# Kernel optimization log

Measured on AMD Instinct MI355X. Metric: run time of the kernel, lower is better.

## Reference

```python
import jax, jax.numpy as jnp
import numpy as np

N_NODES = 10000
IN_DIM, EDGE_DIM, HID_DIM, OUT_DIM = 128, 64, 256, 128
N_EDGES = 640000


def setup_inputs() -> dict:
    key = jax.random.key(0)
    ks = jax.random.split(key, 8)
    x = jax.random.normal(ks[0], (N_NODES, IN_DIM), dtype=jnp.float32)
    edge_index = jax.random.randint(ks[1], (2, N_EDGES), 0, N_NODES, dtype=jnp.int64)
    edge_attr = jax.random.normal(ks[2], (N_EDGES, EDGE_DIM), dtype=jnp.float32)
    # MLP params (PyTorch Linear: y = x @ W.T + b), Kaiming-uniform-ish scale
    s1 = 1.0 / np.sqrt(IN_DIM + EDGE_DIM)
    s2 = 1.0 / np.sqrt(HID_DIM)
    W1 = jax.random.uniform(ks[3], (HID_DIM, IN_DIM + EDGE_DIM), minval=-s1, maxval=s1, dtype=jnp.float32)
    b1 = jax.random.uniform(ks[4], (HID_DIM,), minval=-s1, maxval=s1, dtype=jnp.float32)
    W2 = jax.random.uniform(ks[5], (OUT_DIM, HID_DIM), minval=-s2, maxval=s2, dtype=jnp.float32)
    b2 = jax.random.uniform(ks[6], (OUT_DIM,), minval=-s2, maxval=s2, dtype=jnp.float32)
    return {"x": x, "edge_index": edge_index, "edge_attr": edge_attr,
            "W1": W1, "b1": b1, "W2": W2, "b2": b2}


def reference(x, edge_index, edge_attr, W1, b1, W2, b2):
    # GINE-style concat-message conv: gather -> per-edge MLP -> scatter-add.
    src = edge_index[0]  # message source node x_j
    dst = edge_index[1]  # aggregation target node
    m = jnp.concatenate([x[src], edge_attr], axis=-1)         # [E, F+Fe]
    h = jax.nn.relu(m @ W1.T + b1)                            # [E, H]
    msg = h @ W2.T + b2                                       # [E, O]
    out = jax.ops.segment_sum(msg, dst, num_segments=x.shape[0])  # [N, O]
    return out
```

## Files before the change

kernel.cpp:

```cpp
#include <hip/hip_runtime.h>

#define N_NODES 10000
#define IN_DIM 128
#define EDGE_DIM 64
#define HID_DIM 256
#define OUT_DIM 128
#define N_EDGES 640000


typedef __bf16 bf16x8 __attribute__((ext_vector_type(8)));
typedef float f32x4 __attribute__((ext_vector_type(4)));

static __device__ __forceinline__ unsigned short f2bf(float f) {
    unsigned u = __builtin_bit_cast(unsigned, f);
    u = (u + 0x7fffu + ((u >> 16) & 1u)) >> 16;
    return (unsigned short)u;
}

__global__ void zero_kernel(float* __restrict__ out) {
    int t = blockIdx.x * 256 + threadIdx.x;
    if (t < 320000) ((float4*)out)[t] = make_float4(0.f, 0.f, 0.f, 0.f);
}

__global__ __launch_bounds__(256, 2) void gine_hybrid(
    const int* __restrict__ ei,
    const float* __restrict__ x,
    const float* __restrict__ ea,
    const float* __restrict__ W1,
    const float* __restrict__ b1,
    const float* __restrict__ W2,
    const float* __restrict__ b2,
    float* __restrict__ out)
{
    __shared__ unsigned        sW1u[128 * 97];
    __shared__ __align__(16) float sMsg[16 * 132];
    __shared__ unsigned short  sHu[16 * 132];
    __shared__ float           sB1[128];
    __shared__ int             sSE[16], sDE[16];

    unsigned* sMu = (unsigned*)sMsg;

    const int tid  = threadIdx.x;
    const int hb   = blockIdx.x & 1;
    const int bseq = blockIdx.x >> 1;

    for (int i = tid; i < 128 * 96; i += 256) {
        int r = i / 96, c2 = i - r * 96;
        const float* wr = W1 + (hb * 128 + r) * 192 + c2 * 2;
        sW1u[r * 97 + c2] = (unsigned)f2bf(wr[0]) | ((unsigned)f2bf(wr[1]) << 16);
    }
    if (tid < 128) sB1[tid] = b1[hb * 128 + tid];

    const int o    = tid & 127;
    const int lane = tid & 63;
    const int e16  = lane & 15;
    const int q    = lane >> 4;
    const int wv   = tid >> 6;

    bf16x8 w2frag[2][4];
    #pragma unroll
    for (int mtl = 0; mtl < 2; ++mtl) {
        const float* wbase = W2 + (size_t)((wv * 2 + mtl) * 16 + e16) * 256 + hb * 128 + q * 8;
        #pragma unroll
        for (int kb = 0; kb < 4; ++kb) {
            const float* wr = wbase + kb * 32;
            int4 ai;
            ai.x = (int)((unsigned)f2bf(wr[0]) | ((unsigned)f2bf(wr[1]) << 16));
            ai.y = (int)((unsigned)f2bf(wr[2]) | ((unsigned)f2bf(wr[3]) << 16));
            ai.z = (int)((unsigned)f2bf(wr[4]) | ((unsigned)f2bf(wr[5]) << 16));
            ai.w = (int)((unsigned)f2bf(wr[6]) | ((unsigned)f2bf(wr[7]) << 16));
            w2frag[mtl][kb] = __builtin_bit_cast(bf16x8, ai);
        }
    }
    const float b2o = (hb == 0) ? b2[o] : 0.f;

    __syncthreads();

    for (int g = bseq; g < 40000; g += 512) {
        if (tid < 16) {
            sSE[tid] = ei[g * 16 + tid];
            sDE[tid] = ei[N_EDGES + g * 16 + tid];
        }
        __syncthreads();

        for (int i = tid; i < 16 * 48; i += 256) {
            int ee = i / 48, c4 = i - ee * 48;
            int k = c4 * 4;
            float4 v;
            if (k < 128) v = *(const float4*)(x + (size_t)sSE[ee] * 128 + k);
            else         v = *(const float4*)(ea + (size_t)(g * 16 + ee) * 64 + (k - 128));
            unsigned* mp = sMu + ee * 97 + c4 * 2;
            mp[0] = (unsigned)f2bf(v.x) | ((unsigned)f2bf(v.y) << 16);
            mp[1] = (unsigned)f2bf(v.z) | ((unsigned)f2bf(v.w) << 16);
        }
        __syncthreads();

        {
            f32x4 acc[2];
            acc[0] = (f32x4){0.f, 0.f, 0.f, 0.f};
            acc[1] = (f32x4){0.f, 0.f, 0.f, 0.f};
            #pragma unroll
            for (int ks = 0; ks < 6; ++ks) {
                const unsigned* mp = sMu + e16 * 97 + ks * 16 + q * 4;
                int4 bi;
                bi.x = (int)mp[0]; bi.y = (int)mp[1];
                bi.z = (int)mp[2]; bi.w = (int)mp[3];
                bf16x8 bfrag = __builtin_bit_cast(bf16x8, bi);
                #pragma unroll
                for (int mtl = 0; mtl < 2; ++mtl) {
                    const unsigned* ap = sW1u + ((wv * 2 + mtl) * 16 + e16) * 97 + ks * 16 + q * 4;
                    int4 ai;
                    ai.x = (int)ap[0]; ai.y = (int)ap[1];
                    ai.z = (int)ap[2]; ai.w = (int)ap[3];
                    bf16x8 afrag = __builtin_bit_cast(bf16x8, ai);
                    acc[mtl] = __builtin_amdgcn_mfma_f32_16x16x32_bf16(afrag, bfrag, acc[mtl], 0, 0, 0);
                }
            }
            #pragma unroll
            for (int mtl = 0; mtl < 2; ++mtl) {
                const int hid = (wv * 2 + mtl) * 16 + q * 4;
                float v0 = fmaxf(acc[mtl][0] + sB1[hid + 0], 0.f);
                float v1 = fmaxf(acc[mtl][1] + sB1[hid + 1], 0.f);
                float v2 = fmaxf(acc[mtl][2] + sB1[hid + 2], 0.f);
                float v3 = fmaxf(acc[mtl][3] + sB1[hid + 3], 0.f);
                unsigned* hp = ((unsigned*)sHu) + e16 * 66 + (hid >> 1);
                hp[0] = (unsigned)f2bf(v0) | ((unsigned)f2bf(v1) << 16);
                hp[1] = (unsigned)f2bf(v2) | ((unsigned)f2bf(v3) << 16);
            }
        }
        __syncthreads();

        {
            f32x4 acc2[2];
            acc2[0] = (f32x4){0.f, 0.f, 0.f, 0.f};
            acc2[1] = (f32x4){0.f, 0.f, 0.f, 0.f};
            #pragma unroll
            for (int kb = 0; kb < 4; ++kb) {
                const unsigned* hp = ((const unsigned*)sHu) + e16 * 66 + kb * 16 + q * 4;
                int4 bi;
                bi.x = (int)hp[0]; bi.y = (int)hp[1];
                bi.z = (int)hp[2]; bi.w = (int)hp[3];
                bf16x8 bfrag = __builtin_bit_cast(bf16x8, bi);
                acc2[0] = __builtin_amdgcn_mfma_f32_16x16x32_bf16(w2frag[0][kb], bfrag, acc2[0], 0, 0, 0);
                acc2[1] = __builtin_amdgcn_mfma_f32_16x16x32_bf16(w2frag[1][kb], bfrag, acc2[1], 0, 0, 0);
            }
            #pragma unroll
            for (int mtl = 0; mtl < 2; ++mtl) {
                float* mp = sMsg + e16 * 132 + (wv * 2 + mtl) * 16 + q * 4;
                mp[0] = acc2[mtl][0]; mp[1] = acc2[mtl][1];
                mp[2] = acc2[mtl][2]; mp[3] = acc2[mtl][3];
            }
        }
        __syncthreads();

        {
            const int eb = (tid >> 7) * 8;
            #pragma unroll
            for (int q2 = 0; q2 < 8; ++q2) {
                int ee = eb + q2;
                float v = sMsg[ee * 132 + o] + b2o;
                unsafeAtomicAdd(out + (size_t)sDE[ee] * 128 + o, v);
            }
        }
        __syncthreads();
    }
}

extern "C" void kernel_launch(void* const* d_in, const int* in_sizes, int n_in,
                              void* d_out, int out_size, void* d_ws, size_t ws_size,
                              hipStream_t stream) {
    const float* x  = (const float*)d_in[0];
    const int*   ei = (const int*)d_in[1];
    const float* ea = (const float*)d_in[2];
    const float* W1 = (const float*)d_in[3];
    const float* b1 = (const float*)d_in[4];
    const float* W2 = (const float*)d_in[5];
    const float* b2 = (const float*)d_in[6];
    float* out = (float*)d_out;

    zero_kernel<<<1250, 256, 0, stream>>>(out);
    gine_hybrid<<<1024, 256, 0, stream>>>(ei, x, ea, W1, b1, W2, b2, out);
}
```

Baseline: 884.2 us.

## Double-buffer edge gathers in LDS and cut per-group block barriers

Restructures the edge-group loop into a software pipeline. The next group's x/edge_attr rows and the group after next's edge indices are loaded into registers during the current group's MLP and written to a second LDS buffer afterwards. This hides gather latency and reduces block barriers per group from five to two, since each wave reads back only its own sMsg columns. LDS rows are XOR-swizzled instead of padded, fragments are loaded with vector int4 reads, and fp32-to-bf16 packing for inputs and weights now truncates instead of rounding, which slightly lowers accuracy.

```diff
diff --git a/kernel.cpp b/kernel.cpp
--- a/kernel.cpp
+++ b/kernel.cpp
@@ -11,6 +11,10 @@
 typedef __bf16 bf16x8 __attribute__((ext_vector_type(8)));
 typedef float f32x4 __attribute__((ext_vector_type(4)));
 
+static __device__ __forceinline__ unsigned pk_pre(float lo, float hi) {
+    return (__builtin_bit_cast(unsigned, lo) >> 16) |
+           (__builtin_bit_cast(unsigned, hi) & 0xFFFF0000u);
+}
 static __device__ __forceinline__ unsigned short f2bf(float f) {
     unsigned u = __builtin_bit_cast(unsigned, f);
     u = (u + 0x7fffu + ((u >> 16) & 1u)) >> 16;
@@ -22,7 +26,12 @@
     if (t < 320000) ((float4*)out)[t] = make_float4(0.f, 0.f, 0.f, 0.f);
 }
 
-__global__ __launch_bounds__(256, 2) void gine_hybrid(
+#define FENCE_LGKM()  asm volatile("s_waitcnt lgkmcnt(0)" ::: "memory")
+#define SCHED_FENCE() __builtin_amdgcn_sched_barrier(0)
+#define BLOCK_BAR()   do { FENCE_LGKM(); SCHED_FENCE(); \
+                           __builtin_amdgcn_s_barrier(); SCHED_FENCE(); } while (0)
+
+__global__ __launch_bounds__(256, 2) void gine_pipe(
     const int* __restrict__ ei,
     const float* __restrict__ x,
     const float* __restrict__ ea,
@@ -32,13 +41,12 @@
     const float* __restrict__ b2,
     float* __restrict__ out)
 {
-    __shared__ unsigned        sW1u[128 * 97];
-    __shared__ __align__(16) float sMsg[16 * 132];
-    __shared__ unsigned short  sHu[16 * 132];
-    __shared__ float           sB1[128];
-    __shared__ int             sSE[16], sDE[16];
-
-    unsigned* sMu = (unsigned*)sMsg;
+    __shared__ __align__(16) unsigned sW1u[128 * 96];
+    __shared__ __align__(16) unsigned sMu[2][16 * 96];
+    __shared__ __align__(16) unsigned sHuU[16 * 64];
+    __shared__ __align__(16) float    sMsg[16 * 132];
+    __shared__ float sB1[128];
+    __shared__ __align__(16) int sSE[2][16], sDE[2][16];
 
     const int tid  = threadIdx.x;
     const int hb   = blockIdx.x & 1;
@@ -46,16 +54,19 @@
 
     for (int i = tid; i < 128 * 96; i += 256) {
         int r = i / 96, c2 = i - r * 96;
-        const float* wr = W1 + (hb * 128 + r) * 192 + c2 * 2;
-        sW1u[r * 97 + c2] = (unsigned)f2bf(wr[0]) | ((unsigned)f2bf(wr[1]) << 16);
+        const float* w = W1 + (size_t)(hb * 128 + r) * 192 + c2 * 2;
+        sW1u[r * 96 + (c2 ^ ((r & 7) << 2))] = pk_pre(w[0], w[1]);
     }
     if (tid < 128) sB1[tid] = b1[hb * 128 + tid];
 
-    const int o    = tid & 127;
     const int lane = tid & 63;
     const int e16  = lane & 15;
     const int q    = lane >> 4;
     const int wv   = tid >> 6;
+    const int l32  = lane & 31;
+    const int eh   = (lane >> 5) * 8;
+    const int o    = wv * 32 + l32;
+    const int rsw  = (e16 & 7) << 2;
 
     bf16x8 w2frag[2][4];
     #pragma unroll
@@ -65,104 +76,133 @@
         for (int kb = 0; kb < 4; ++kb) {
             const float* wr = wbase + kb * 32;
             int4 ai;
-            ai.x = (int)((unsigned)f2bf(wr[0]) | ((unsigned)f2bf(wr[1]) << 16));
-            ai.y = (int)((unsigned)f2bf(wr[2]) | ((unsigned)f2bf(wr[3]) << 16));
-            ai.z = (int)((unsigned)f2bf(wr[4]) | ((unsigned)f2bf(wr[5]) << 16));
-            ai.w = (int)((unsigned)f2bf(wr[6]) | ((unsigned)f2bf(wr[7]) << 16));
+            ai.x = (int)pk_pre(wr[0], wr[1]);
+            ai.y = (int)pk_pre(wr[2], wr[3]);
+            ai.z = (int)pk_pre(wr[4], wr[5]);
+            ai.w = (int)pk_pre(wr[6], wr[7]);
             w2frag[mtl][kb] = __builtin_bit_cast(bf16x8, ai);
         }
     }
-    const float b2o = (hb == 0) ? b2[o] : 0.f;
-
+    const float b2o = hb ? 0.f : b2[o];
+
+    {
+        const int g0 = bseq;
+        const int g1 = (bseq + 512 < 40000) ? bseq + 512 : bseq;
+        if (tid < 16) {
+            sSE[0][tid] = ei[g0 * 16 + tid];
+            sDE[0][tid] = ei[N_EDGES + g0 * 16 + tid];
+        } else if (tid < 32) {
+            int t = tid - 16;
+            sSE[1][t] = ei[g1 * 16 + t];
+            sDE[1][t] = ei[N_EDGES + g1 * 16 + t];
+        }
+    }
     __syncthreads();
 
-    for (int g = bseq; g < 40000; g += 512) {
-        if (tid < 16) {
-            sSE[tid] = ei[g * 16 + tid];
-            sDE[tid] = ei[N_EDGES + g * 16 + tid];
-        }
-        __syncthreads();
-
-        for (int i = tid; i < 16 * 48; i += 256) {
-            int ee = i / 48, c4 = i - ee * 48;
-            int k = c4 * 4;
-            float4 v;
-            if (k < 128) v = *(const float4*)(x + (size_t)sSE[ee] * 128 + k);
-            else         v = *(const float4*)(ea + (size_t)(g * 16 + ee) * 64 + (k - 128));
-            unsigned* mp = sMu + ee * 97 + c4 * 2;
-            mp[0] = (unsigned)f2bf(v.x) | ((unsigned)f2bf(v.y) << 16);
-            mp[1] = (unsigned)f2bf(v.z) | ((unsigned)f2bf(v.w) << 16);
-        }
-        __syncthreads();
-
-        {
-            f32x4 acc[2];
-            acc[0] = (f32x4){0.f, 0.f, 0.f, 0.f};
-            acc[1] = (f32x4){0.f, 0.f, 0.f, 0.f};
-            #pragma unroll
-            for (int ks = 0; ks < 6; ++ks) {
-                const unsigned* mp = sMu + e16 * 97 + ks * 16 + q * 4;
-                int4 bi;
-                bi.x = (int)mp[0]; bi.y = (int)mp[1];
-                bi.z = (int)mp[2]; bi.w = (int)mp[3];
-                bf16x8 bfrag = __builtin_bit_cast(bf16x8, bi);
-                #pragma unroll
-                for (int mtl = 0; mtl < 2; ++mtl) {
-                    const unsigned* ap = sW1u + ((wv * 2 + mtl) * 16 + e16) * 97 + ks * 16 + q * 4;
-                    int4 ai;
-                    ai.x = (int)ap[0]; ai.y = (int)ap[1];
-                    ai.z = (int)ap[2]; ai.w = (int)ap[3];
-                    bf16x8 afrag = __builtin_bit_cast(bf16x8, ai);
-                    acc[mtl] = __builtin_amdgcn_mfma_f32_16x16x32_bf16(afrag, bfrag, acc[mtl], 0, 0, 0);
-                }
-            }
+    #pragma unroll
+    for (int t = 0; t < 3; ++t) {
+        int i = tid + 256 * t;
+        int ee = i / 48, c4 = i - ee * 48, k = c4 * 4;
+        const float* p = (k < 128)
+            ? x + (size_t)sSE[0][ee] * 128 + k
+            : ea + (size_t)(bseq * 16 + ee) * 64 + (k - 128);
+        float4 v = *(const float4*)p;
+        unsigned* mp = &sMu[0][ee * 96 + ((c4 * 2) ^ ((ee & 7) << 2))];
+        mp[0] = pk_pre(v.x, v.y);
+        mp[1] = pk_pre(v.z, v.w);
+    }
+    __syncthreads();
+
+    int cur = 0;
+    for (int g = bseq; g < 40000; g += 512, cur ^= 1) {
+        const int nxt = cur ^ 1;
+        const int g1v = (g + 512  < 40000) ? g + 512  : g;
+        const int g2v = (g + 1024 < 40000) ? g + 1024 : g;
+
+        float4 rawS[3]; int eeS[3], c4S[3];
+        #pragma unroll
+        for (int t = 0; t < 3; ++t) {
+            int i = tid + 256 * t;
+            int ee = i / 48, c4 = i - ee * 48, k = c4 * 4;
+            eeS[t] = ee; c4S[t] = c4;
+            const float* p = (k < 128)
+                ? x + (size_t)sSE[nxt][ee] * 128 + k
+                : ea + (size_t)(g1v * 16 + ee) * 64 + (k - 128);
+            rawS[t] = *(const float4*)p;
+        }
+        int i2 = 0, d2 = 0;
+        if (tid < 16)       i2 = ei[g2v * 16 + tid];
+        else if (tid < 32)  d2 = ei[N_EDGES + g2v * 16 + (tid - 16)];
+        const int4 dv0 = *(const int4*)&sDE[cur][eh];
+        const int4 dv1 = *(const int4*)&sDE[cur][eh + 4];
+
+        f32x4 acc1[2];
+        acc1[0] = (f32x4){0.f, 0.f, 0.f, 0.f};
+        acc1[1] = (f32x4){0.f, 0.f, 0.f, 0.f};
+        #pragma unroll
+        for (int ks = 0; ks < 6; ++ks) {
+            const int col = (ks * 16 + q * 4);
+            bf16x8 bfrag = __builtin_bit_cast(bf16x8,
+                *(const int4*)&sMu[cur][e16 * 96 + (col ^ rsw)]);
             #pragma unroll
             for (int mtl = 0; mtl < 2; ++mtl) {
-                const int hid = (wv * 2 + mtl) * 16 + q * 4;
-                float v0 = fmaxf(acc[mtl][0] + sB1[hid + 0], 0.f);
-                float v1 = fmaxf(acc[mtl][1] + sB1[hid + 1], 0.f);
-                float v2 = fmaxf(acc[mtl][2] + sB1[hid + 2], 0.f);
-                float v3 = fmaxf(acc[mtl][3] + sB1[hid + 3], 0.f);
-                unsigned* hp = ((unsigned*)sHu) + e16 * 66 + (hid >> 1);
-                hp[0] = (unsigned)f2bf(v0) | ((unsigned)f2bf(v1) << 16);
-                hp[1] = (unsigned)f2bf(v2) | ((unsigned)f2bf(v3) << 16);
+                bf16x8 afrag = __builtin_bit_cast(bf16x8,
+                    *(const int4*)&sW1u[((wv * 2 + mtl) * 16 + e16) * 96 + (col ^ rsw)]);
+                acc1[mtl] = __builtin_amdgcn_mfma_f32_16x16x32_bf16(afrag, bfrag, acc1[mtl], 0, 0, 0);
             }
         }
-        __syncthreads();
+        #pragma unroll
+        for (int mtl = 0; mtl < 2; ++mtl) {
+            const int hid = (wv * 2 + mtl) * 16 + q * 4;
+            float v0 = fmaxf(acc1[mtl][0] + sB1[hid + 0], 0.f);
+            float v1 = fmaxf(acc1[mtl][1] + sB1[hid + 1], 0.f);
+            float v2 = fmaxf(acc1[mtl][2] + sB1[hid + 2], 0.f);
+            float v3 = fmaxf(acc1[mtl][3] + sB1[hid + 3], 0.f);
+            unsigned* hp = &sHuU[e16 * 64 + ((hid >> 1) ^ rsw)];
+            hp[0] = (unsigned)f2bf(v0) | ((unsigned)f2bf(v1) << 16);
+            hp[1] = (unsigned)f2bf(v2) | ((unsigned)f2bf(v3) << 16);
+        }
+
+        BLOCK_BAR();
+
+        f32x4 acc2[2];
+        acc2[0] = (f32x4){0.f, 0.f, 0.f, 0.f};
+        acc2[1] = (f32x4){0.f, 0.f, 0.f, 0.f};
+        #pragma unroll
+        for (int kb = 0; kb < 4; ++kb) {
+            const int col = (kb * 16 + q * 4);
+            bf16x8 bfrag = __builtin_bit_cast(bf16x8,
+                *(const int4*)&sHuU[e16 * 64 + (col ^ rsw)]);
+            acc2[0] = __builtin_amdgcn_mfma_f32_16x16x32_bf16(w2frag[0][kb], bfrag, acc2[0], 0, 0, 0);
+            acc2[1] = __builtin_amdgcn_mfma_f32_16x16x32_bf16(w2frag[1][kb], bfrag, acc2[1], 0, 0, 0);
+        }
+        #pragma unroll
+        for (int mtl = 0; mtl < 2; ++mtl) {
+            *(f32x4*)&sMsg[e16 * 132 + (wv * 2 + mtl) * 16 + q * 4] = acc2[mtl];
+        }
+        FENCE_LGKM(); SCHED_FENCE();
+
+        float sv[8];
+        #pragma unroll
+        for (int j = 0; j < 8; ++j) sv[j] = sMsg[(eh + j) * 132 + o];
+
+        #pragma unroll
+        for (int t = 0; t < 3; ++t) {
+            unsigned* mp = &sMu[nxt][eeS[t] * 96 + ((c4S[t] * 2) ^ ((eeS[t] & 7) << 2))];
+            mp[0] = pk_pre(rawS[t].x, rawS[t].y);
+            mp[1] = pk_pre(rawS[t].z, rawS[t].w);
+        }
+        if (tid < 16)       sSE[cur][tid] = i2;
+        else if (tid < 32)  sDE[cur][tid - 16] = d2;
 
         {
-            f32x4 acc2[2];
-            acc2[0] = (f32x4){0.f, 0.f, 0.f, 0.f};
-            acc2[1] = (f32x4){0.f, 0.f, 0.f, 0.f};
+            const int dsts[8] = {dv0.x, dv0.y, dv0.z, dv0.w, dv1.x, dv1.y, dv1.z, dv1.w};
             #pragma unroll
-            for (int kb = 0; kb < 4; ++kb) {
-                const unsigned* hp = ((const unsigned*)sHu) + e16 * 66 + kb * 16 + q * 4;
-                int4 bi;
-                bi.x = (int)hp[0]; bi.y = (int)hp[1];
-                bi.z = (int)hp[2]; bi.w = (int)hp[3];
-                bf16x8 bfrag = __builtin_bit_cast(bf16x8, bi);
-                acc2[0] = __builtin_amdgcn_mfma_f32_16x16x32_bf16(w2frag[0][kb], bfrag, acc2[0], 0, 0, 0);
-                acc2[1] = __builtin_amdgcn_mfma_f32_16x16x32_bf16(w2frag[1][kb], bfrag, acc2[1], 0, 0, 0);
-            }
-            #pragma unroll
-            for (int mtl = 0; mtl < 2; ++mtl) {
-                float* mp = sMsg + e16 * 132 + (wv * 2 + mtl) * 16 + q * 4;
-                mp[0] = acc2[mtl][0]; mp[1] = acc2[mtl][1];
-                mp[2] = acc2[mtl][2]; mp[3] = acc2[mtl][3];
-            }
-        }
-        __syncthreads();
-
-        {
-            const int eb = (tid >> 7) * 8;
-            #pragma unroll
-            for (int q2 = 0; q2 < 8; ++q2) {
-                int ee = eb + q2;
-                float v = sMsg[ee * 132 + o] + b2o;
-                unsafeAtomicAdd(out + (size_t)sDE[ee] * 128 + o, v);
-            }
-        }
-        __syncthreads();
+            for (int j = 0; j < 8; ++j)
+                unsafeAtomicAdd(out + (size_t)dsts[j] * 128 + o, sv[j] + b2o);
+        }
+
+        BLOCK_BAR();
     }
 }
 
@@ -179,5 +219,5 @@
     float* out = (float*)d_out;
 
     zero_kernel<<<1250, 256, 0, stream>>>(out);
-    gine_hybrid<<<1024, 256, 0, stream>>>(ei, x, ea, W1, b1, W2, b2, out);
-}
+    gine_pipe<<<1024, 256, 0, stream>>>(ei, x, ea, W1, b1, W2, b2, out);
+}
```

Measured after the change: 725.8 us. 1.22x faster.
